# Kernel optimization log

Measured on AMD Instinct MI355X. Metric: run time of the kernel, lower is better.

The kernel has to match this reference:

```python
import jax, jax.numpy as jnp
import numpy as np

NUM_HEADS = 16


def setup_inputs() -> dict:
    key = jax.random.key(0)
    ks = jax.random.split(key, 5)
    B, S, H = 2, 2048, 1024
    scale = 0.02
    return {
        "x": jax.random.normal(ks[0], (B, S, H), dtype=jnp.float32),
        "w_qkv": jax.random.normal(ks[1], (H, 3 * H), dtype=jnp.float32) * scale,
        "b_qkv": jax.random.normal(ks[2], (3 * H,), dtype=jnp.float32) * scale,
        "w_out": jax.random.normal(ks[3], (H, H), dtype=jnp.float32) * scale,
        "b_out": jax.random.normal(ks[4], (H,), dtype=jnp.float32) * scale,
    }


def reference(x, w_qkv, b_qkv, w_out, b_out):
    B, S, H = x.shape
    nh = NUM_HEADS
    hd = H // nh
    attn_scale = 1.0 / np.sqrt(hd).astype(np.float32)

    qkv = x @ w_qkv + b_qkv                       # (B, S, 3H)
    q, k, v = jnp.split(qkv, 3, axis=-1)
    # (B, S, H) -> (B, nh, S, hd)
    to_heads = lambda t: t.reshape(B, S, nh, hd).transpose(0, 2, 1, 3)
    q, k, v = to_heads(q), to_heads(k), to_heads(v)

    scores = jnp.einsum("bhid,bhjd->bhij", q, k) * attn_scale  # (B, nh, S, S)
    # Source masks where triu(ones)==0 -> strictly-lower triangle masked;
    # allowed positions are j >= i (attends to present and future).
    i = jnp.arange(S)[:, None]
    j = jnp.arange(S)[None, :]
    scores = jnp.where(j >= i, scores, -jnp.inf)
    attn = jax.nn.softmax(scores, axis=-1)        # dropout is identity (eval)

    out = jnp.einsum("bhij,bhjd->bhid", attn, v)  # (B, nh, S, hd)
    out = out.transpose(0, 2, 1, 3).reshape(B, S, H)
    return out @ w_out + b_out
```

## Files before the change

kernel.cpp:

```cpp
#include <hip/hip_runtime.h>
#include <hip/hip_bf16.h>
#include <stdint.h>
#include <stddef.h>

typedef __bf16 bf16_t;
typedef __bf16 bf16x4 __attribute__((ext_vector_type(4)));
typedef __bf16 bf16x8 __attribute__((ext_vector_type(8)));
typedef float f32x4 __attribute__((ext_vector_type(4)));

#define MFMA16(a, b, c) __builtin_amdgcn_mfma_f32_16x16x32_bf16(a, b, c, 0, 0, 0)

#define SEQ 2048
#define NHEAD 16
#define HD 64
#define HID 1024
#define QKV_LD 3072
#define VT_LD 2080

__global__ void cast_f32_bf16(const float* __restrict__ in,
                              bf16_t* __restrict__ out, int n) {
    int i = (blockIdx.x * 256 + threadIdx.x) * 4;
    if (i < n) {
        float4 v = *(const float4*)(in + i);
        bf16x4 o = {(bf16_t)v.x, (bf16_t)v.y, (bf16_t)v.z, (bf16_t)v.w};
        *(bf16x4*)(out + i) = o;
    }
}

__global__ void transpose_cast(const float* __restrict__ W,
                               bf16_t* __restrict__ Wt, int K, int N) {
    __shared__ bf16_t tile[32][33];
    int n0 = blockIdx.x * 32, k0 = blockIdx.y * 32;
    int tx = threadIdx.x, ty = threadIdx.y;
#pragma unroll
    for (int i = 0; i < 4; i++)
        tile[ty + i * 8][tx] = (bf16_t)W[(size_t)(k0 + ty + i * 8) * N + n0 + tx];
    __syncthreads();
#pragma unroll
    for (int i = 0; i < 4; i++)
        Wt[(size_t)(n0 + ty + i * 8) * K + k0 + tx] = tile[tx][ty + i * 8];
}

__global__ __launch_bounds__(256)
void vt_transpose(const bf16_t* __restrict__ qkv, bf16_t* __restrict__ Vt) {
    int s0 = blockIdx.x * 64;
    int bh = blockIdx.y;
    int b = bh >> 4, h = bh & 15;
    int tid = threadIdx.x;
    __shared__ __align__(16) bf16_t tile[64][72];

    int row = tid >> 3, c8 = (tid & 7) * 8;
#pragma unroll
    for (int it = 0; it < 2; it++) {
        int sr = row + it * 32;
        bf16x8 v = *(const bf16x8*)(qkv + ((size_t)b * SEQ + s0 + sr) * QKV_LD +
                                    2 * HID + h * HD + c8);
        *(bf16x8*)(&tile[sr][c8]) = v;
    }
    __syncthreads();
#pragma unroll
    for (int it = 0; it < 2; it++) {
        int d = row + it * 32;
        bf16x8 w;
#pragma unroll
        for (int e = 0; e < 8; e++) w[e] = tile[c8 + e][d];
        *(bf16x8*)(Vt + ((size_t)bh * HD + d) * VT_LD + s0 + c8) = w;
    }
}

template <typename OutT>
__global__ __launch_bounds__(256)
void gemm_bt_bias(const bf16_t* __restrict__ A, const bf16_t* __restrict__ Bt,
                  const float* __restrict__ bias, OutT* __restrict__ C,
                  int M, int N, int K) {
    constexpr int LDA = 40;
    __shared__ __align__(16) bf16_t As[128][LDA];
    __shared__ __align__(16) bf16_t Bs[128][LDA];

    int m0 = blockIdx.y * 128;
    int n0 = blockIdx.x * 128;
    int tid = threadIdx.x;
    int wave = tid >> 6, lane = tid & 63;
    int quad = lane >> 4, l16 = lane & 15;
    int wm = (wave >> 1) * 64, wn = (wave & 1) * 64;

    f32x4 acc[4][4] = {};

    int sr = tid >> 2;
    int sc = (tid & 3) * 8;

    for (int k0 = 0; k0 < K; k0 += 32) {
        bf16x8 a0 = *(const bf16x8*)(A + (size_t)(m0 + sr) * K + k0 + sc);
        bf16x8 a1 = *(const bf16x8*)(A + (size_t)(m0 + 64 + sr) * K + k0 + sc);
        bf16x8 b0 = *(const bf16x8*)(Bt + (size_t)(n0 + sr) * K + k0 + sc);
        bf16x8 b1 = *(const bf16x8*)(Bt + (size_t)(n0 + 64 + sr) * K + k0 + sc);
        *(bf16x8*)(&As[sr][sc]) = a0;
        *(bf16x8*)(&As[64 + sr][sc]) = a1;
        *(bf16x8*)(&Bs[sr][sc]) = b0;
        *(bf16x8*)(&Bs[64 + sr][sc]) = b1;
        __syncthreads();

        bf16x8 af[4], bfr[4];
#pragma unroll
        for (int t = 0; t < 4; t++)
            af[t] = *(const bf16x8*)(&As[wm + t * 16 + l16][quad * 8]);
#pragma unroll
        for (int t = 0; t < 4; t++)
            bfr[t] = *(const bf16x8*)(&Bs[wn + t * 16 + l16][quad * 8]);
#pragma unroll
        for (int mt = 0; mt < 4; mt++)
#pragma unroll
            for (int nt = 0; nt < 4; nt++)
                acc[mt][nt] = MFMA16(af[mt], bfr[nt], acc[mt][nt]);
        __syncthreads();
    }

#pragma unroll
    for (int mt = 0; mt < 4; mt++) {
        int row = m0 + wm + mt * 16 + quad * 4;
#pragma unroll
        for (int nt = 0; nt < 4; nt++) {
            int col = n0 + wn + nt * 16 + l16;
            float bv = bias[col];
#pragma unroll
            for (int r = 0; r < 4; r++)
                C[(size_t)(row + r) * N + col] = (OutT)(acc[mt][nt][r] + bv);
        }
    }
}

__global__ __launch_bounds__(256)
void attn_kernel(const bf16_t* __restrict__ qkv, const bf16_t* __restrict__ Vt,
                 bf16_t* __restrict__ attn_out) {
    int L = blockIdx.y * 16 + blockIdx.x;
    int xcd = L & 7, idx = L >> 3;
    int bh = xcd + 8 * (idx >> 4);
    int xb = idx & 15;
    int b = bh >> 4, h = bh & 15;

    int tid = threadIdx.x, wave = tid >> 6, lane = tid & 63;
    int quad = lane >> 4, l16 = lane & 15;

    const bf16_t* q_g = qkv + (size_t)b * SEQ * QKV_LD + (size_t)h * HD;
    const bf16_t* k_g = q_g + HID;
    const bf16_t* vt_g = Vt + (size_t)bh * HD * VT_LD;

    __shared__ __align__(16) bf16_t Ks[64][72];
    __shared__ __align__(16) bf16_t Vs[64][72];
    __shared__ __align__(16) bf16_t Ps[4][16][72];

    bf16x8 ones;
#pragma unroll
    for (int e = 0; e < 8; e++) ones[e] = (bf16_t)1.0f;

    int srow = tid >> 3, sc8 = (tid & 7) * 8;

#pragma unroll
    for (int phase = 0; phase < 2; phase++) {
        int tile = phase ? (31 - xb) : xb;
        int i0 = tile * 64;
        int iw = i0 + wave * 16;

        bf16x8 qa0 = *(const bf16x8*)(q_g + (size_t)(iw + l16) * QKV_LD + quad * 8);
        bf16x8 qa1 = *(const bf16x8*)(q_g + (size_t)(iw + l16) * QKV_LD + 32 + quad * 8);

        f32x4 o[4] = {};
        f32x4 lacc = {};

        for (int j0 = i0; j0 < SEQ; j0 += 64) {
            __syncthreads();
            bf16x8 k0 = *(const bf16x8*)(k_g + (size_t)(j0 + srow) * QKV_LD + sc8);
            bf16x8 k1 = *(const bf16x8*)(k_g + (size_t)(j0 + 32 + srow) * QKV_LD + sc8);
            bf16x8 v0 = *(const bf16x8*)(vt_g + (size_t)srow * VT_LD + j0 + sc8);
            bf16x8 v1 = *(const bf16x8*)(vt_g + (size_t)(32 + srow) * VT_LD + j0 + sc8);
            *(bf16x8*)(&Ks[srow][sc8]) = k0;
            *(bf16x8*)(&Ks[32 + srow][sc8]) = k1;
            *(bf16x8*)(&Vs[srow][sc8]) = v0;
            *(bf16x8*)(&Vs[32 + srow][sc8]) = v1;
            __syncthreads();

            f32x4 s[4];
#pragma unroll
            for (int jt = 0; jt < 4; jt++) {
                bf16x8 kb0 = *(const bf16x8*)(&Ks[jt * 16 + l16][quad * 8]);
                bf16x8 kb1 = *(const bf16x8*)(&Ks[jt * 16 + l16][32 + quad * 8]);
                f32x4 a = {};
                a = MFMA16(qa0, kb0, a);
                a = MFMA16(qa1, kb1, a);
                s[jt] = a;
            }

#pragma unroll
            for (int jt = 0; jt < 4; jt++) {
                int gj = j0 + jt * 16 + l16;
#pragma unroll
                for (int r = 0; r < 4; r++) {
                    int gi = iw + quad * 4 + r;
                    float p = (gj >= gi) ? __expf(s[jt][r] * 0.125f) : 0.0f;
                    Ps[wave][quad * 4 + r][jt * 16 + l16] = (bf16_t)p;
                }
            }

            bf16x8 pa0 = *(const bf16x8*)(&Ps[wave][l16][quad * 8]);
            bf16x8 pa1 = *(const bf16x8*)(&Ps[wave][l16][32 + quad * 8]);

            lacc = MFMA16(pa0, ones, lacc);
            lacc = MFMA16(pa1, ones, lacc);

#pragma unroll
            for (int nt = 0; nt < 4; nt++) {
                bf16x8 vb0 = *(const bf16x8*)(&Vs[nt * 16 + l16][quad * 8]);
                bf16x8 vb1 = *(const bf16x8*)(&Vs[nt * 16 + l16][32 + quad * 8]);
                o[nt] = MFMA16(pa0, vb0, o[nt]);
                o[nt] = MFMA16(pa1, vb1, o[nt]);
            }
        }

#pragma unroll
        for (int r = 0; r < 4; r++) {
            int gi = iw + quad * 4 + r;
            float inv = 1.0f / lacc[r];
#pragma unroll
            for (int nt = 0; nt < 4; nt++)
                attn_out[(size_t)(b * SEQ + gi) * HID + h * HD + nt * 16 + l16] =
                    (bf16_t)(o[nt][r] * inv);
        }
    }
}

extern "C" void kernel_launch(void* const* d_in, const int* in_sizes, int n_in,
                              void* d_out, int out_size, void* d_ws, size_t ws_size,
                              hipStream_t stream) {
    const float* x     = (const float*)d_in[0];
    const float* w_qkv = (const float*)d_in[1];
    const float* b_qkv = (const float*)d_in[2];
    const float* w_out = (const float*)d_in[3];
    const float* b_out = (const float*)d_in[4];
    float* out = (float*)d_out;

    char* ws = (char*)d_ws;
    bf16_t* xbf   = (bf16_t*)(ws);
    bf16_t* Vt    = (bf16_t*)(ws);
    bf16_t* wqkvT = (bf16_t*)(ws + 8388608);
    bf16_t* woutT = (bf16_t*)(ws + 14680064);
    bf16_t* qkv   = (bf16_t*)(ws + 16777216);
    bf16_t* attn  = (bf16_t*)(ws + 41943040);

    cast_f32_bf16<<<4096, 256, 0, stream>>>(x, xbf, 4096 * 1024);

    transpose_cast<<<dim3(3072 / 32, 1024 / 32), dim3(32, 8), 0, stream>>>(
        w_qkv, wqkvT, 1024, 3072);
    transpose_cast<<<dim3(1024 / 32, 1024 / 32), dim3(32, 8), 0, stream>>>(
        w_out, woutT, 1024, 1024);

    gemm_bt_bias<bf16_t><<<dim3(3072 / 128, 4096 / 128), 256, 0, stream>>>(
        xbf, wqkvT, b_qkv, qkv, 4096, 3072, 1024);

    vt_transpose<<<dim3(SEQ / 64, 2 * NHEAD), 256, 0, stream>>>(qkv, Vt);

    attn_kernel<<<dim3(16, 2 * NHEAD), 256, 0, stream>>>(qkv, Vt, attn);

    gemm_bt_bias<float><<<dim3(1024 / 128, 4096 / 128), 256, 0, stream>>>(
        attn, woutT, b_out, out, 4096, 1024, 1024);
}
```

Before: 208.1 us.

## Use direct global-to-LDS loads in GEMM and widen attention KV tiles to 128

The GEMM now stages A and B tiles with global_load_lds intrinsics into unpadded shared arrays, skipping the register round-trip. The attention kernel processes 128 keys per iteration instead of 64, which halves the number of barrier-separated loads and raises the MFMA work per sync. The cost is more shared memory and registers, possible bank conflicts in the unpadded GEMM tiles, and extra masked work because each key loop now starts at a 128-aligned boundary below the diagonal.

```diff
diff --git a/kernel.cpp b/kernel.cpp
--- a/kernel.cpp
+++ b/kernel.cpp
@@ -9,6 +9,11 @@
 typedef float f32x4 __attribute__((ext_vector_type(4)));
 
 #define MFMA16(a, b, c) __builtin_amdgcn_mfma_f32_16x16x32_bf16(a, b, c, 0, 0, 0)
+
+#define GLL16(g, l)                                                      \
+    __builtin_amdgcn_global_load_lds(                                    \
+        (const __attribute__((address_space(1))) void*)(g),              \
+        (__attribute__((address_space(3))) void*)(l), 16, 0, 0)
 
 #define SEQ 2048
 #define NHEAD 16
@@ -73,9 +78,8 @@
 void gemm_bt_bias(const bf16_t* __restrict__ A, const bf16_t* __restrict__ Bt,
                   const float* __restrict__ bias, OutT* __restrict__ C,
                   int M, int N, int K) {
-    constexpr int LDA = 40;
-    __shared__ __align__(16) bf16_t As[128][LDA];
-    __shared__ __align__(16) bf16_t Bs[128][LDA];
+    __shared__ __align__(16) bf16_t As[128][32];
+    __shared__ __align__(16) bf16_t Bs[128][32];
 
     int m0 = blockIdx.y * 128;
     int n0 = blockIdx.x * 128;
@@ -86,18 +90,16 @@
 
     f32x4 acc[4][4] = {};
 
-    int sr = tid >> 2;
-    int sc = (tid & 3) * 8;
+    const bf16_t* a_base = A + (size_t)(m0 + wave * 32 + (lane >> 2)) * K + (lane & 3) * 8;
+    const bf16_t* b_base = Bt + (size_t)(n0 + wave * 32 + (lane >> 2)) * K + (lane & 3) * 8;
+    bf16_t* as_base = &As[wave * 32][0];
+    bf16_t* bs_base = &Bs[wave * 32][0];
 
     for (int k0 = 0; k0 < K; k0 += 32) {
-        bf16x8 a0 = *(const bf16x8*)(A + (size_t)(m0 + sr) * K + k0 + sc);
-        bf16x8 a1 = *(const bf16x8*)(A + (size_t)(m0 + 64 + sr) * K + k0 + sc);
-        bf16x8 b0 = *(const bf16x8*)(Bt + (size_t)(n0 + sr) * K + k0 + sc);
-        bf16x8 b1 = *(const bf16x8*)(Bt + (size_t)(n0 + 64 + sr) * K + k0 + sc);
-        *(bf16x8*)(&As[sr][sc]) = a0;
-        *(bf16x8*)(&As[64 + sr][sc]) = a1;
-        *(bf16x8*)(&Bs[sr][sc]) = b0;
-        *(bf16x8*)(&Bs[64 + sr][sc]) = b1;
+        GLL16(a_base + k0, as_base);
+        GLL16(a_base + 16 * K + k0, as_base + 16 * 32);
+        GLL16(b_base + k0, bs_base);
+        GLL16(b_base + 16 * K + k0, bs_base + 16 * 32);
         __syncthreads();
 
         bf16x8 af[4], bfr[4];
@@ -145,15 +147,16 @@
     const bf16_t* k_g = q_g + HID;
     const bf16_t* vt_g = Vt + (size_t)bh * HD * VT_LD;
 
-    __shared__ __align__(16) bf16_t Ks[64][72];
-    __shared__ __align__(16) bf16_t Vs[64][72];
-    __shared__ __align__(16) bf16_t Ps[4][16][72];
+    __shared__ __align__(16) bf16_t Ks[128][72];
+    __shared__ __align__(16) bf16_t Vs[64][136];
+    __shared__ __align__(16) bf16_t Ps[4][16][136];
 
     bf16x8 ones;
 #pragma unroll
     for (int e = 0; e < 8; e++) ones[e] = (bf16_t)1.0f;
 
-    int srow = tid >> 3, sc8 = (tid & 7) * 8;
+    int krow = tid >> 3, kc8 = (tid & 7) * 8;
+    int vrow = tid >> 4, vc8 = (tid & 15) * 8;
 
 #pragma unroll
     for (int phase = 0; phase < 2; phase++) {
@@ -167,21 +170,23 @@
         f32x4 o[4] = {};
         f32x4 lacc = {};
 
-        for (int j0 = i0; j0 < SEQ; j0 += 64) {
+        for (int j0 = i0 & ~127; j0 < SEQ; j0 += 128) {
             __syncthreads();
-            bf16x8 k0 = *(const bf16x8*)(k_g + (size_t)(j0 + srow) * QKV_LD + sc8);
-            bf16x8 k1 = *(const bf16x8*)(k_g + (size_t)(j0 + 32 + srow) * QKV_LD + sc8);
-            bf16x8 v0 = *(const bf16x8*)(vt_g + (size_t)srow * VT_LD + j0 + sc8);
-            bf16x8 v1 = *(const bf16x8*)(vt_g + (size_t)(32 + srow) * VT_LD + j0 + sc8);
-            *(bf16x8*)(&Ks[srow][sc8]) = k0;
-            *(bf16x8*)(&Ks[32 + srow][sc8]) = k1;
-            *(bf16x8*)(&Vs[srow][sc8]) = v0;
-            *(bf16x8*)(&Vs[32 + srow][sc8]) = v1;
+#pragma unroll
+            for (int t = 0; t < 4; t++) {
+                bf16x8 kv = *(const bf16x8*)(k_g + (size_t)(j0 + krow + t * 32) * QKV_LD + kc8);
+                *(bf16x8*)(&Ks[krow + t * 32][kc8]) = kv;
+            }
+#pragma unroll
+            for (int t = 0; t < 4; t++) {
+                bf16x8 vv = *(const bf16x8*)(vt_g + (size_t)(vrow + t * 16) * VT_LD + j0 + vc8);
+                *(bf16x8*)(&Vs[vrow + t * 16][vc8]) = vv;
+            }
             __syncthreads();
 
-            f32x4 s[4];
-#pragma unroll
-            for (int jt = 0; jt < 4; jt++) {
+            f32x4 s[8];
+#pragma unroll
+            for (int jt = 0; jt < 8; jt++) {
                 bf16x8 kb0 = *(const bf16x8*)(&Ks[jt * 16 + l16][quad * 8]);
                 bf16x8 kb1 = *(const bf16x8*)(&Ks[jt * 16 + l16][32 + quad * 8]);
                 f32x4 a = {};
@@ -191,7 +196,7 @@
             }
 
 #pragma unroll
-            for (int jt = 0; jt < 4; jt++) {
+            for (int jt = 0; jt < 8; jt++) {
                 int gj = j0 + jt * 16 + l16;
 #pragma unroll
                 for (int r = 0; r < 4; r++) {
@@ -201,18 +206,20 @@
                 }
             }
 
-            bf16x8 pa0 = *(const bf16x8*)(&Ps[wave][l16][quad * 8]);
-            bf16x8 pa1 = *(const bf16x8*)(&Ps[wave][l16][32 + quad * 8]);
-
-            lacc = MFMA16(pa0, ones, lacc);
-            lacc = MFMA16(pa1, ones, lacc);
+            bf16x8 pa[4];
+#pragma unroll
+            for (int kk = 0; kk < 4; kk++) {
+                pa[kk] = *(const bf16x8*)(&Ps[wave][l16][kk * 32 + quad * 8]);
+                lacc = MFMA16(pa[kk], ones, lacc);
+            }
 
 #pragma unroll
             for (int nt = 0; nt < 4; nt++) {
-                bf16x8 vb0 = *(const bf16x8*)(&Vs[nt * 16 + l16][quad * 8]);
-                bf16x8 vb1 = *(const bf16x8*)(&Vs[nt * 16 + l16][32 + quad * 8]);
-                o[nt] = MFMA16(pa0, vb0, o[nt]);
-                o[nt] = MFMA16(pa1, vb1, o[nt]);
+#pragma unroll
+                for (int kk = 0; kk < 4; kk++) {
+                    bf16x8 vb = *(const bf16x8*)(&Vs[nt * 16 + l16][kk * 32 + quad * 8]);
+                    o[nt] = MFMA16(pa[kk], vb, o[nt]);
+                }
             }
         }
 
```

After: 205.9 us. About the same (-1.0%).
